# Kernel tuning notes

Measured on AMD Instinct MI355X. Metric: run time of the kernel, lower is better.

Reference implementation:

```python
import jax, jax.numpy as jnp
import numpy as np
import math

VOCAB = 32000
D = 2048
H = 16
KVH = 4
HD = D // H          # 128
FF = 5632
L = 2
S = 2048
B = 1
EPS = 1e-5
ROPE_BASE = 10000.0


def setup_inputs() -> dict:
    key = jax.random.key(0)
    ks = jax.random.split(key, 12)
    sc = 0.02
    # RoPE table: [S, HD//2, 2] (cos, sin), matching precompute_freqs_cis
    inv = 1.0 / (ROPE_BASE ** (jnp.arange(0, HD, 2, dtype=jnp.float32) / HD))
    pos = jnp.arange(S, dtype=jnp.float32)
    f = jnp.outer(pos, inv)
    freqs_cis = jnp.stack([jnp.cos(f), jnp.sin(f)], axis=-1)
    mask = jnp.tril(jnp.ones((S, S), dtype=bool))
    return {
        "input_ids": jax.random.randint(ks[0], (B, S), 0, VOCAB, dtype=jnp.int32),
        "mask": mask,
        "freqs_cis": freqs_cis,
        "w_embed": jax.random.normal(ks[1], (VOCAB, D), jnp.float32) * sc,
        "wqkv": jax.random.normal(ks[2], (L, D, D + 2 * KVH * HD), jnp.float32) * sc,
        "wo": jax.random.normal(ks[3], (L, D, D), jnp.float32) * sc,
        "w1": jax.random.normal(ks[4], (L, D, FF), jnp.float32) * sc,
        "w3": jax.random.normal(ks[5], (L, D, FF), jnp.float32) * sc,
        "w2": jax.random.normal(ks[6], (L, FF, D), jnp.float32) * sc,
        "attn_norm_w": jnp.ones((L, D), jnp.float32),
        "ff_norm_w": jnp.ones((L, D), jnp.float32),
        "final_norm_w": jnp.ones((D,), jnp.float32),
        "w_head": jax.random.normal(ks[7], (D, VOCAB), jnp.float32) * sc,
    }


def _rmsnorm(x, w):
    xf = x.astype(jnp.float32)
    n = xf * jax.lax.rsqrt(jnp.mean(xf * xf, axis=-1, keepdims=True) + EPS)
    return n.astype(x.dtype) * w


def _rope(x, fc):
    # x: [b, h, s, hd]; fc: [s, hd/2, 2]
    xr = x.reshape(*x.shape[:-1], HD // 2, 2)
    cos, sin = fc[..., 0], fc[..., 1]  # [s, hd/2] broadcast over b,h
    out = jnp.stack([xr[..., 0] * cos - xr[..., 1] * sin,
                     xr[..., 1] * cos + xr[..., 0] * sin], axis=-1)
    return out.reshape(x.shape).astype(x.dtype)


def _attention(x, mask, fc, wqkv, wo):
    b, s, _ = x.shape
    qkv = x @ wqkv  # [b, s, D + 2*kv_dim]
    kv_dim = KVH * HD
    q, k, v = jnp.split(qkv, [D, D + kv_dim], axis=-1)
    q = q.reshape(b, s, H, HD).transpose(0, 2, 1, 3)      # [b,H,s,hd]
    k = k.reshape(b, s, KVH, HD).transpose(0, 2, 1, 3)    # [b,KVH,s,hd]
    v = v.reshape(b, s, KVH, HD).transpose(0, 2, 1, 3)
    q = _rope(q, fc)
    k = _rope(k, fc)
    rep = H // KVH
    k = jnp.repeat(k, rep, axis=1)  # [b,H,s,hd]
    v = jnp.repeat(v, rep, axis=1)
    scores = jnp.einsum('bhqd,bhkd->bhqk', q, k) / math.sqrt(HD)
    scores = jnp.where(mask, scores, -1e30)
    attn = jax.nn.softmax(scores, axis=-1)
    out = jnp.einsum('bhqk,bhkd->bhqd', attn, v)
    out = out.transpose(0, 2, 1, 3).reshape(b, s, D)
    return out @ wo


def reference(input_ids, mask, freqs_cis, w_embed, wqkv, wo, w1, w3, w2,
              attn_norm_w, ff_norm_w, final_norm_w, w_head):
    x = w_embed[input_ids]  # [B,S,D]
    for l in range(L):
        h = x + _attention(_rmsnorm(x, attn_norm_w[l]), mask, freqs_cis,
                           wqkv[l], wo[l])
        hn = _rmsnorm(h, ff_norm_w[l])
        x = h + (jax.nn.silu(hn @ w1[l]) * (hn @ w3[l])) @ w2[l]
    x = _rmsnorm(x, final_norm_w)
    return x @ w_head  # [B,S,VOCAB]
```

## Files before the change

### kernel.cpp

```cpp
#include <hip/hip_runtime.h>

#define DD 2048
#define SEQ 2048
#define NH 16
#define NKV 4
#define HD 128
#define FFD 5632
#define NL 2

typedef __bf16 bf16x8 __attribute__((ext_vector_type(8)));
typedef float f32x4 __attribute__((ext_vector_type(4)));

__device__ __forceinline__ unsigned short f2bf(float f) {
    unsigned int u = __builtin_bit_cast(unsigned int, f);
    u += 0x7fffu + ((u >> 16) & 1u);
    return (unsigned short)(u >> 16);
}

__global__ __launch_bounds__(256)
void embed_gather(const int* __restrict__ ids, const float* __restrict__ wemb,
                  float* __restrict__ x)
{
    int s = blockIdx.x;
    int id = ids[s];
    const float4* src = (const float4*)(wemb + (size_t)id * DD);
    float4* dst = (float4*)(x + (size_t)s * DD);
    dst[threadIdx.x] = src[threadIdx.x];
    dst[threadIdx.x + 256] = src[threadIdx.x + 256];
}

__global__ __launch_bounds__(256)
void rmsnorm_bf16(const float* __restrict__ x, const float* __restrict__ w,
                  unsigned short* __restrict__ out)
{
    int row = blockIdx.x;
    int t = threadIdx.x;
    const float4* xr = (const float4*)(x + (size_t)row * DD);
    float4 v0 = xr[t], v1 = xr[t + 256];
    float ss = v0.x * v0.x + v0.y * v0.y + v0.z * v0.z + v0.w * v0.w
             + v1.x * v1.x + v1.y * v1.y + v1.z * v1.z + v1.w * v1.w;
#pragma unroll
    for (int off = 32; off; off >>= 1) ss += __shfl_down(ss, off);
    __shared__ float red[4];
    if ((t & 63) == 0) red[t >> 6] = ss;
    __syncthreads();
    float sc = rsqrtf((red[0] + red[1] + red[2] + red[3]) * (1.0f / DD) + 1e-5f);
    const float4* wr = (const float4*)w;
    float4 w0 = wr[t], w1v = wr[t + 256];
    ushort4 o0, o1;
    o0.x = f2bf(v0.x * sc * w0.x);  o0.y = f2bf(v0.y * sc * w0.y);
    o0.z = f2bf(v0.z * sc * w0.z);  o0.w = f2bf(v0.w * sc * w0.w);
    o1.x = f2bf(v1.x * sc * w1v.x); o1.y = f2bf(v1.y * sc * w1v.y);
    o1.z = f2bf(v1.z * sc * w1v.z); o1.w = f2bf(v1.w * sc * w1v.w);
    ushort4* op = (ushort4*)(out + (size_t)row * DD);
    op[t] = o0;
    op[t + 256] = o1;
}

__global__ __launch_bounds__(256)
void transpose_cast(const float* __restrict__ src, unsigned short* __restrict__ dst,
                    int ld_src, int ld_dst, size_t sb, size_t db)
{
    __shared__ float tile[64][65];
    src += (size_t)blockIdx.z * sb;
    dst += (size_t)blockIdx.z * db;
    int c0 = blockIdx.x * 64, r0 = blockIdx.y * 64;
    int tx = threadIdx.x & 15, ty = threadIdx.x >> 4;
#pragma unroll
    for (int i = 0; i < 4; ++i) {
        int r = ty + i * 16;
        float4 v = *(const float4*)(src + (size_t)(r0 + r) * ld_src + c0 + tx * 4);
        tile[r][tx * 4 + 0] = v.x; tile[r][tx * 4 + 1] = v.y;
        tile[r][tx * 4 + 2] = v.z; tile[r][tx * 4 + 3] = v.w;
    }
    __syncthreads();
#pragma unroll
    for (int i = 0; i < 4; ++i) {
        int c = ty + i * 16;
        ushort4 o;
        o.x = f2bf(tile[tx * 4 + 0][c]); o.y = f2bf(tile[tx * 4 + 1][c]);
        o.z = f2bf(tile[tx * 4 + 2][c]); o.w = f2bf(tile[tx * 4 + 3][c]);
        *(ushort4*)(dst + (size_t)(c0 + c) * ld_dst + r0 + tx * 4) = o;
    }
}

__global__ void rope_qk(const float* __restrict__ qkv, const float* __restrict__ fc,
                        unsigned short* __restrict__ Qb, unsigned short* __restrict__ Kb)
{
    int s = blockIdx.x;
    int hh = blockIdx.y;
    int i = threadIdx.x;
    float2 cs = *(const float2*)(fc + ((size_t)s * 64 + i) * 2);
    const float* src;
    unsigned short* dst;
    if (hh < NH) {
        src = qkv + (size_t)s * 3072 + hh * HD;
        dst = Qb + ((size_t)hh * SEQ + s) * HD;
    } else {
        int kh = hh - NH;
        src = qkv + (size_t)s * 3072 + DD + kh * HD;
        dst = Kb + ((size_t)kh * SEQ + s) * HD;
    }
    float2 xv = *(const float2*)(src + 2 * i);
    ushort2 o;
    o.x = f2bf(xv.x * cs.x - xv.y * cs.y);
    o.y = f2bf(xv.y * cs.x + xv.x * cs.y);
    *(ushort2*)(dst + 2 * i) = o;
}

__global__ __launch_bounds__(256)
void silu_mul(const float* __restrict__ h, unsigned short* __restrict__ g)
{
    size_t i = (size_t)blockIdx.x * 256 + threadIdx.x;
    size_t row = i / (FFD / 4), c4 = i % (FFD / 4);
    const float* p = h + row * (2 * FFD) + c4 * 4;
    float4 a = *(const float4*)(p);
    float4 b = *(const float4*)(p + FFD);
    ushort4 o;
    o.x = f2bf(a.x / (1.f + __expf(-a.x)) * b.x);
    o.y = f2bf(a.y / (1.f + __expf(-a.y)) * b.y);
    o.z = f2bf(a.z / (1.f + __expf(-a.z)) * b.z);
    o.w = f2bf(a.w / (1.f + __expf(-a.w)) * b.w);
    *(ushort4*)(g + row * FFD + c4 * 4) = o;
}

__global__ __launch_bounds__(256)
void gemm_bf16(const unsigned short* __restrict__ A, const unsigned short* __restrict__ B,
               float* __restrict__ C, const float* __restrict__ Res,
               int N, int K, int mT)
{
    __shared__ __attribute__((aligned(16))) unsigned char smem[65536];
    const int tid = threadIdx.x;
    const int lane = tid & 63;
    const int w = tid >> 6;
    const int nwg = gridDim.x;
    const int qq = nwg >> 3;
    const int logical = ((int)blockIdx.x & 7) * qq + ((int)blockIdx.x >> 3);
    const int m0 = (logical % mT) * 128;
    const int n0 = (logical / mT) * 128;
    const int wm = (w >> 1) * 64, wn = (w & 1) * 64;
    const int lrow = lane & 15, lgrp = lane >> 4;
    const int NT = K >> 6;

    f32x4 acc[4][4];
#pragma unroll
    for (int i = 0; i < 4; ++i)
#pragma unroll
        for (int j = 0; j < 4; ++j) acc[i][j] = 0.f;

    auto stage = [&](int bsel, int kt) {
#pragma unroll
        for (int it = 0; it < 4; ++it) {
            int o = it * 4096 + tid * 16;
            int row = o >> 7;
            int col = (o & 127) ^ ((row & 7) << 4);
            const char* ga = (const char*)A + ((size_t)(m0 + row) * K + kt) * 2 + col;
            const char* gb = (const char*)B + ((size_t)(n0 + row) * K + kt) * 2 + col;
            __builtin_amdgcn_global_load_lds(
                (__attribute__((address_space(1))) const void*)ga,
                (__attribute__((address_space(3))) void*)(smem + bsel * 32768 + it * 4096 + w * 1024),
                16, 0, 0);
            __builtin_amdgcn_global_load_lds(
                (__attribute__((address_space(1))) const void*)gb,
                (__attribute__((address_space(3))) void*)(smem + bsel * 32768 + 16384 + it * 4096 + w * 1024),
                16, 0, 0);
        }
    };

    stage(0, 0);
    int cur = 0;
    for (int t = 0; t < NT; ++t) {
        if (t + 1 < NT) {
            stage(cur ^ 1, (t + 1) << 6);
            asm volatile("s_waitcnt vmcnt(8)" ::: "memory");
        } else {
            asm volatile("s_waitcnt vmcnt(0)" ::: "memory");
        }
        __builtin_amdgcn_s_barrier();
        __builtin_amdgcn_sched_barrier(0);
        const unsigned char* buf = smem + cur * 32768;
#pragma unroll
        for (int kk = 0; kk < 2; ++kk) {
            bf16x8 af[4], bfr[4];
            int cb = kk * 64 + lgrp * 16;
#pragma unroll
            for (int i = 0; i < 4; ++i) {
                int ra = wm + i * 16 + lrow;
                af[i] = *(const bf16x8*)(buf + ra * 128 + (cb ^ ((ra & 7) << 4)));
                int rb = wn + i * 16 + lrow;
                bfr[i] = *(const bf16x8*)(buf + 16384 + rb * 128 + (cb ^ ((rb & 7) << 4)));
            }
#pragma unroll
            for (int i = 0; i < 4; ++i)
#pragma unroll
                for (int j = 0; j < 4; ++j)
                    acc[i][j] = __builtin_amdgcn_mfma_f32_16x16x32_bf16(af[i], bfr[j], acc[i][j], 0, 0, 0);
        }
        __builtin_amdgcn_s_barrier();
        cur ^= 1;
    }

    const bool hasRes = (Res != nullptr);
#pragma unroll
    for (int i = 0; i < 4; ++i)
#pragma unroll
        for (int j = 0; j < 4; ++j) {
            int r = m0 + wm + i * 16 + lgrp * 4;
            int c = n0 + wn + j * 16 + lrow;
#pragma unroll
            for (int jj = 0; jj < 4; ++jj) {
                size_t idx = (size_t)(r + jj) * N + c;
                float v = acc[i][j][jj];
                if (hasRes) v += Res[idx];
                C[idx] = v;
            }
        }
}

__global__ __launch_bounds__(512, 1)
void gemm_bf16_256(const unsigned short* __restrict__ A, const unsigned short* __restrict__ B,
                   float* __restrict__ C, int N, int K, int mT)
{
    __shared__ __attribute__((aligned(16))) unsigned char smem[131072];
    const int tid = threadIdx.x;
    const int lane = tid & 63;
    const int w = tid >> 6;
    const int nwg = gridDim.x;
    const int qq = nwg >> 3;
    const int logical = ((int)blockIdx.x & 7) * qq + ((int)blockIdx.x >> 3);
    const int m0 = (logical % mT) * 256;
    const int n0 = (logical / mT) * 256;
    const int wm2 = (w >> 2) * 128;
    const int wn4 = (w & 3) * 64;
    const int lrow = lane & 15, lgrp = lane >> 4;
    const int NT = K >> 6;

    f32x4 acc[8][4];
#pragma unroll
    for (int i = 0; i < 8; ++i)
#pragma unroll
        for (int j = 0; j < 4; ++j) acc[i][j] = 0.f;

    auto stage_all = [&](int bsel, int kt) {
#pragma unroll
        for (int it = 0; it < 8; ++it) {
            int o = (it & 3) * 8192 + tid * 16;
            int row = o >> 7;
            int col = (o & 127) ^ ((row & 7) << 4);
            const unsigned short* base = (it < 4) ? A : B;
            int r0 = (it < 4) ? m0 : n0;
            const char* g = (const char*)base + ((size_t)(r0 + row) * K + kt) * 2 + col;
            __builtin_amdgcn_global_load_lds(
                (__attribute__((address_space(1))) const void*)g,
                (__attribute__((address_space(3))) void*)(smem + bsel * 65536 +
                    (it < 4 ? 0 : 32768) + (it & 3) * 8192 + w * 1024),
                16, 0, 0);
        }
    };

    stage_all(0, 0);
    int cur = 0;
    for (int t = 0; t < NT; ++t) {
        if (t + 1 < NT) {
            stage_all(cur ^ 1, (t + 1) << 6);
            asm volatile("s_waitcnt vmcnt(8)" ::: "memory");
        } else {
            asm volatile("s_waitcnt vmcnt(0)" ::: "memory");
        }
        __builtin_amdgcn_s_barrier();
        __builtin_amdgcn_sched_barrier(0);
        const unsigned char* buf = smem + cur * 65536;

        bf16x8 bfr[4][2];
#pragma unroll
        for (int nj = 0; nj < 4; ++nj)
#pragma unroll
            for (int kk = 0; kk < 2; ++kk) {
                int rb = wn4 + nj * 16 + lrow;
                int cb = kk * 64 + lgrp * 16;
                bfr[nj][kk] = *(const bf16x8*)(buf + 32768 + rb * 128 + (cb ^ ((rb & 7) << 4)));
            }
#pragma unroll
        for (int mp = 0; mp < 4; ++mp) {
            bf16x8 afr[2][2];
#pragma unroll
            for (int i = 0; i < 2; ++i)
#pragma unroll
                for (int kk = 0; kk < 2; ++kk) {
                    int ra = wm2 + (mp * 2 + i) * 16 + lrow;
                    int cb = kk * 64 + lgrp * 16;
                    afr[i][kk] = *(const bf16x8*)(buf + ra * 128 + (cb ^ ((ra & 7) << 4)));
                }
            __builtin_amdgcn_s_setprio(1);
#pragma unroll
            for (int i = 0; i < 2; ++i)
#pragma unroll
                for (int nj = 0; nj < 4; ++nj)
#pragma unroll
                    for (int kk = 0; kk < 2; ++kk)
                        acc[mp * 2 + i][nj] = __builtin_amdgcn_mfma_f32_16x16x32_bf16(
                            afr[i][kk], bfr[nj][kk], acc[mp * 2 + i][nj], 0, 0, 0);
            __builtin_amdgcn_s_setprio(0);
        }
        __builtin_amdgcn_s_barrier();
        cur ^= 1;
    }

#pragma unroll
    for (int mi = 0; mi < 8; ++mi)
#pragma unroll
        for (int nj = 0; nj < 4; ++nj) {
            int r = m0 + wm2 + mi * 16 + lgrp * 4;
            int c = n0 + wn4 + nj * 16 + lrow;
#pragma unroll
            for (int jj = 0; jj < 4; ++jj)
                C[(size_t)(r + jj) * N + c] = acc[mi][nj][jj];
        }
}

__global__ __launch_bounds__(256)
void attn_fwd(const unsigned short* __restrict__ Qb, const unsigned short* __restrict__ Kb,
              const unsigned short* __restrict__ VTb, unsigned short* __restrict__ O)
{
    __shared__ __attribute__((aligned(16))) unsigned char smem[73728];
    const int qb = 31 - (int)blockIdx.x;
    const int h = blockIdx.y;
    const int kvh = h >> 2;
    const int tid = threadIdx.x, lane = tid & 63, w = tid >> 6;
    const int lrow = lane & 15, lgrp = lane >> 4;
    const int q0 = qb * 64 + w * 16;

    bf16x8 qf[4];
    const unsigned short* qrow = Qb + ((size_t)h * SEQ + q0 + lrow) * HD;
#pragma unroll
    for (int c = 0; c < 4; ++c)
        qf[c] = *(const bf16x8*)(qrow + c * 32 + lgrp * 8);

    float m[4], l[4];
    f32x4 oacc[8];
#pragma unroll
    for (int j = 0; j < 8; ++j) oacc[j] = 0.f;
#pragma unroll
    for (int j = 0; j < 4; ++j) { m[j] = -3.0e38f; l[j] = 0.f; }

    const float scale = 0.08838834764831845f;
    const char* kbase = (const char*)(Kb + (size_t)kvh * SEQ * HD);
    const char* vbase = (const char*)(VTb + (size_t)kvh * HD * SEQ);
    unsigned char* Pl = smem + 65536 + w * 2048;

    auto stage_kv = [&](int bsel, int t) {
#pragma unroll
        for (int it = 0; it < 4; ++it) {
            int o = it * 4096 + tid * 16;
            int row = o >> 8, col = o & 255;
            int scol = col ^ ((row & 7) << 4);
            const char* g = kbase + (size_t)(t * 64 + row) * 256 + scol;
            __builtin_amdgcn_global_load_lds(
                (__attribute__((address_space(1))) const void*)g,
                (__attribute__((address_space(3))) void*)(smem + bsel * 32768 + it * 4096 + w * 1024),
                16, 0, 0);
        }
#pragma unroll
        for (int it = 0; it < 4; ++it) {
            int o = it * 4096 + tid * 16;
            int row = o >> 7, col = o & 127;
            int scol = col ^ ((row & 7) << 4);
            const char* g = vbase + (size_t)row * (SEQ * 2) + (size_t)t * 128 + scol;
            __builtin_amdgcn_global_load_lds(
                (__attribute__((address_space(1))) const void*)g,
                (__attribute__((address_space(3))) void*)(smem + bsel * 32768 + 16384 + it * 4096 + w * 1024),
                16, 0, 0);
        }
    };

    stage_kv(0, 0);
    int cur = 0;
    for (int t = 0; t <= qb; ++t) {
        if (t < qb) {
            stage_kv(cur ^ 1, t + 1);
            asm volatile("s_waitcnt vmcnt(8)" ::: "memory");
        } else {
            asm volatile("s_waitcnt vmcnt(0)" ::: "memory");
        }
        __builtin_amdgcn_s_barrier();
        __builtin_amdgcn_sched_barrier(0);
        const unsigned char* kb = smem + cur * 32768;
        const unsigned char* vtb = kb + 16384;

        f32x4 sf[4];
#pragma unroll
        for (int kf = 0; kf < 4; ++kf) sf[kf] = 0.f;
#pragma unroll
        for (int kf = 0; kf < 4; ++kf) {
            int rb = kf * 16 + lrow;
            int rbase = rb * 256;
            int sw = (rb & 7) << 4;
#pragma unroll
            for (int c = 0; c < 4; ++c) {
                bf16x8 kfr = *(const bf16x8*)(kb + rbase + ((c * 64 + lgrp * 16) ^ sw));
                sf[kf] = __builtin_amdgcn_mfma_f32_16x16x32_bf16(qf[c], kfr, sf[kf], 0, 0, 0);
            }
        }
        const bool diag = (t == qb);
        float mx[4] = {-3.0e38f, -3.0e38f, -3.0e38f, -3.0e38f};
#pragma unroll
        for (int kf = 0; kf < 4; ++kf)
#pragma unroll
            for (int j = 0; j < 4; ++j) {
                float v = sf[kf][j] * scale;
                if (diag && (t * 64 + kf * 16 + lrow) > (q0 + lgrp * 4 + j)) v = -3.0e38f;
                sf[kf][j] = v;
                mx[j] = fmaxf(mx[j], v);
            }
#pragma unroll
        for (int off = 1; off < 16; off <<= 1)
#pragma unroll
            for (int j = 0; j < 4; ++j) mx[j] = fmaxf(mx[j], __shfl_xor(mx[j], off));
        float alpha[4], rs[4];
#pragma unroll
        for (int j = 0; j < 4; ++j) {
            float mn = fmaxf(m[j], mx[j]);
            alpha[j] = __expf(m[j] - mn);
            m[j] = mn;
            rs[j] = 0.f;
        }
#pragma unroll
        for (int kf = 0; kf < 4; ++kf)
#pragma unroll
            for (int j = 0; j < 4; ++j) {
                float p = __expf(sf[kf][j] - m[j]);
                rs[j] += p;
                int qq = lgrp * 4 + j;
                int addr = qq * 128 + (((kf * 16 + lrow) * 2) ^ ((qq & 7) << 4));
                *(unsigned short*)(Pl + addr) = f2bf(p);
            }
#pragma unroll
        for (int off = 1; off < 16; off <<= 1)
#pragma unroll
            for (int j = 0; j < 4; ++j) rs[j] += __shfl_xor(rs[j], off);
#pragma unroll
        for (int j = 0; j < 4; ++j) l[j] = l[j] * alpha[j] + rs[j];
#pragma unroll
        for (int hf = 0; hf < 8; ++hf)
#pragma unroll
            for (int j = 0; j < 4; ++j) oacc[hf][j] *= alpha[j];
#pragma unroll
        for (int c = 0; c < 2; ++c) {
            int cb = c * 64 + lgrp * 16;
            bf16x8 pf = *(const bf16x8*)(Pl + lrow * 128 + (cb ^ ((lrow & 7) << 4)));
#pragma unroll
            for (int hf = 0; hf < 8; ++hf) {
                int rv = hf * 16 + lrow;
                bf16x8 vf = *(const bf16x8*)(vtb + rv * 128 + (cb ^ ((rv & 7) << 4)));
                oacc[hf] = __builtin_amdgcn_mfma_f32_16x16x32_bf16(pf, vf, oacc[hf], 0, 0, 0);
            }
        }
        __builtin_amdgcn_s_barrier();
        cur ^= 1;
    }
#pragma unroll
    for (int hf = 0; hf < 8; ++hf)
#pragma unroll
        for (int j = 0; j < 4; ++j) {
            float v = oacc[hf][j] / l[j];
            int qg = q0 + lgrp * 4 + j;
            O[(size_t)qg * DD + h * HD + hf * 16 + lrow] = f2bf(v);
        }
}

extern "C" void kernel_launch(void* const* d_in, const int* in_sizes, int n_in,
                              void* d_out, int out_size, void* d_ws, size_t ws_size,
                              hipStream_t stream)
{
    (void)in_sizes; (void)n_in; (void)out_size; (void)ws_size;
    const int* ids = (const int*)d_in[0];
    const float* fc   = (const float*)d_in[2];
    const float* wemb = (const float*)d_in[3];
    const float* wqkv = (const float*)d_in[4];
    const float* wo   = (const float*)d_in[5];
    const float* w1   = (const float*)d_in[6];
    const float* w3   = (const float*)d_in[7];
    const float* w2   = (const float*)d_in[8];
    const float* anw  = (const float*)d_in[9];
    const float* fnw  = (const float*)d_in[10];
    const float* finw = (const float*)d_in[11];
    const float* wh   = (const float*)d_in[12];
    float* out = (float*)d_out;
    char* ws = (char*)d_ws;

    unsigned short* WQKVT = (unsigned short*)(ws);
    unsigned short* WOT   = (unsigned short*)(ws + 25165824);
    unsigned short* W13T  = (unsigned short*)(ws + 41943040);
    unsigned short* W2T   = (unsigned short*)(ws + 134217728);
    unsigned short* WHT   = (unsigned short*)(ws + 180355072);
    float*          X     = (float*)(ws + 311427072);
    unsigned short* XN    = (unsigned short*)(ws + 328204288);
    float*          QKV   = (float*)(ws + 336592896);
    unsigned short* Qb    = (unsigned short*)(ws + 361758720);
    unsigned short* Kb    = (unsigned short*)(ws + 370147328);
    unsigned short* VT    = (unsigned short*)(ws + 372244480);
    unsigned short* AO    = (unsigned short*)(ws + 374341632);
    float*          H13   = (float*)(ws + 382730240);
    unsigned short* G     = (unsigned short*)(ws + 475004928);

    transpose_cast<<<dim3(48, 32, 2), 256, 0, stream>>>(wqkv, WQKVT, 3072, 2048,
        (size_t)2048 * 3072, (size_t)3072 * 2048);
    transpose_cast<<<dim3(32, 32, 2), 256, 0, stream>>>(wo, WOT, 2048, 2048,
        (size_t)2048 * 2048, (size_t)2048 * 2048);
    transpose_cast<<<dim3(88, 32, 2), 256, 0, stream>>>(w1, W13T, 5632, 2048,
        (size_t)2048 * 5632, (size_t)11264 * 2048);
    transpose_cast<<<dim3(88, 32, 2), 256, 0, stream>>>(w3, W13T + (size_t)5632 * 2048, 5632, 2048,
        (size_t)2048 * 5632, (size_t)11264 * 2048);
    transpose_cast<<<dim3(32, 88, 2), 256, 0, stream>>>(w2, W2T, 2048, 5632,
        (size_t)5632 * 2048, (size_t)2048 * 5632);
    transpose_cast<<<dim3(500, 32, 1), 256, 0, stream>>>(wh, WHT, 32000, 2048, 0, 0);

    embed_gather<<<dim3(SEQ), 256, 0, stream>>>(ids, wemb, X);

    for (int lyr = 0; lyr < NL; ++lyr) {
        const unsigned short* wqkvT_l = WQKVT + (size_t)lyr * 3072 * 2048;
        const unsigned short* woT_l   = WOT   + (size_t)lyr * 2048 * 2048;
        const unsigned short* w13T_l  = W13T  + (size_t)lyr * 11264 * 2048;
        const unsigned short* w2T_l   = W2T   + (size_t)lyr * 2048 * 5632;

        rmsnorm_bf16<<<dim3(SEQ), 256, 0, stream>>>(X, anw + lyr * DD, XN);
        gemm_bf16<<<dim3(24 * 16), 256, 0, stream>>>(XN, wqkvT_l, QKV, nullptr, 3072, 2048, 16);
        rope_qk<<<dim3(SEQ, NH + NKV), 64, 0, stream>>>(QKV, fc, Qb, Kb);
        transpose_cast<<<dim3(2, 32, 4), 256, 0, stream>>>(QKV + 2560, VT, 3072, 2048,
            128, (size_t)128 * 2048);
        attn_fwd<<<dim3(32, NH), 256, 0, stream>>>(Qb, Kb, VT, AO);
        gemm_bf16<<<dim3(16 * 16), 256, 0, stream>>>(AO, woT_l, X, X, 2048, 2048, 16);
        rmsnorm_bf16<<<dim3(SEQ), 256, 0, stream>>>(X, fnw + lyr * DD, XN);
        gemm_bf16_256<<<dim3(8 * 44), 512, 0, stream>>>(XN, w13T_l, H13, 11264, 2048, 8);
        silu_mul<<<dim3(11264), 256, 0, stream>>>(H13, G);
        gemm_bf16<<<dim3(16 * 16), 256, 0, stream>>>(G, w2T_l, X, X, 2048, 5632, 16);
    }
    rmsnorm_bf16<<<dim3(SEQ), 256, 0, stream>>>(X, finw, XN);
    gemm_bf16_256<<<dim3(8 * 125), 512, 0, stream>>>(XN, WHT, out, 32000, 2048, 8);
}
```

Baseline: 1.283 ms.

## Restructure 256-tile GEMM into four-stage K=32 pipeline with split staging

The 256x256 bf16 GEMM main loop changes from a double-buffered K=64 tile to a four-buffer K=32 ring with three tiles in flight. A and B loads are issued separately, with B loads placed in the middle of the compute phase, and a new LDS swizzle packs two rows per 128-byte line. A second barrier splits the MFMA work into two halves. The goal is deeper prefetch and better overlap of global-to-LDS traffic with MFMA work, at the cost of more barriers per K-step and trickier vmcnt bookkeeping.

Result: no change. 1.276 ms (-0.5%).

```diff
diff --git a/kernel.cpp b/kernel.cpp
--- a/kernel.cpp
+++ b/kernel.cpp
@@ -10,6 +10,9 @@
 
 typedef __bf16 bf16x8 __attribute__((ext_vector_type(8)));
 typedef float f32x4 __attribute__((ext_vector_type(4)));
+
+#define AS1 __attribute__((address_space(1)))
+#define AS3 __attribute__((address_space(3)))
 
 __device__ __forceinline__ unsigned short f2bf(float f) {
     unsigned int u = __builtin_bit_cast(unsigned int, f);
@@ -157,12 +160,12 @@
             const char* ga = (const char*)A + ((size_t)(m0 + row) * K + kt) * 2 + col;
             const char* gb = (const char*)B + ((size_t)(n0 + row) * K + kt) * 2 + col;
             __builtin_amdgcn_global_load_lds(
-                (__attribute__((address_space(1))) const void*)ga,
-                (__attribute__((address_space(3))) void*)(smem + bsel * 32768 + it * 4096 + w * 1024),
+                (AS1 const void*)ga,
+                (AS3 void*)(smem + bsel * 32768 + it * 4096 + w * 1024),
                 16, 0, 0);
             __builtin_amdgcn_global_load_lds(
-                (__attribute__((address_space(1))) const void*)gb,
-                (__attribute__((address_space(3))) void*)(smem + bsel * 32768 + 16384 + it * 4096 + w * 1024),
+                (AS1 const void*)gb,
+                (AS3 void*)(smem + bsel * 32768 + 16384 + it * 4096 + w * 1024),
                 16, 0, 0);
         }
     };
@@ -231,9 +234,8 @@
     const int m0 = (logical % mT) * 256;
     const int n0 = (logical / mT) * 256;
     const int wm2 = (w >> 2) * 128;
-    const int wn4 = (w & 3) * 64;
-    const int lrow = lane & 15, lgrp = lane >> 4;
-    const int NT = K >> 6;
+    const int lrow = lane & 15, lgrp = (lane >> 4) & 3;
+    const int NT = K >> 5;
 
     f32x4 acc[8][4];
 #pragma unroll
@@ -241,69 +243,69 @@
 #pragma unroll
         for (int j = 0; j < 4; ++j) acc[i][j] = 0.f;
 
-    auto stage_all = [&](int bsel, int kt) {
-#pragma unroll
-        for (int it = 0; it < 8; ++it) {
-            int o = (it & 3) * 8192 + tid * 16;
-            int row = o >> 7;
-            int col = (o & 127) ^ ((row & 7) << 4);
-            const unsigned short* base = (it < 4) ? A : B;
-            int r0 = (it < 4) ? m0 : n0;
-            const char* g = (const char*)base + ((size_t)(r0 + row) * K + kt) * 2 + col;
+    const int X = (((lrow & 1) << 6) | (lgrp << 4)) ^ ((lrow >> 1) << 4);
+    const int aoff = ((wm2 >> 1) + (lrow >> 1)) * 128 + X;
+    const int boff = 16384 + (((w & 3) * 32) + (lrow >> 1)) * 128 + X;
+
+    auto stage_part = [&](int ktile, int part) {
+        const unsigned short* base = part ? B : A;
+        const int r0 = part ? n0 : m0;
+        const int ktb = ktile << 6;
+#pragma unroll
+        for (int j = 0; j < 2; ++j) {
+            int o = j * 8192 + tid * 16;
+            int p = o >> 7;
+            int sl = (o & 127) ^ ((p & 7) << 4);
+            int r = 2 * p + (sl >> 6);
+            int cb = sl & 63;
+            const char* g = (const char*)base + (size_t)(r0 + r) * K * 2 + ktb + cb;
             __builtin_amdgcn_global_load_lds(
-                (__attribute__((address_space(1))) const void*)g,
-                (__attribute__((address_space(3))) void*)(smem + bsel * 65536 +
-                    (it < 4 ? 0 : 32768) + (it & 3) * 8192 + w * 1024),
+                (AS1 const void*)g,
+                (AS3 void*)(smem + (ktile & 3) * 32768 + part * 16384 + o),
                 16, 0, 0);
         }
     };
 
-    stage_all(0, 0);
-    int cur = 0;
+#pragma unroll
+    for (int p0 = 0; p0 < 3; ++p0) { stage_part(p0, 0); stage_part(p0, 1); }
+
     for (int t = 0; t < NT; ++t) {
-        if (t + 1 < NT) {
-            stage_all(cur ^ 1, (t + 1) << 6);
-            asm volatile("s_waitcnt vmcnt(8)" ::: "memory");
-        } else {
-            asm volatile("s_waitcnt vmcnt(0)" ::: "memory");
-        }
+        const unsigned char* buf = smem + (t & 3) * 32768;
+        const bool have3 = (t + 3 < NT);
+        if (have3) stage_part(t + 3, 0);
+        if (have3)              asm volatile("s_waitcnt vmcnt(10)" ::: "memory");
+        else if (t + 2 < NT)    asm volatile("s_waitcnt vmcnt(8)"  ::: "memory");
+        else if (t + 1 < NT)    asm volatile("s_waitcnt vmcnt(4)"  ::: "memory");
+        else                    asm volatile("s_waitcnt vmcnt(0)"  ::: "memory");
         __builtin_amdgcn_s_barrier();
         __builtin_amdgcn_sched_barrier(0);
-        const unsigned char* buf = smem + cur * 65536;
-
-        bf16x8 bfr[4][2];
-#pragma unroll
-        for (int nj = 0; nj < 4; ++nj)
-#pragma unroll
-            for (int kk = 0; kk < 2; ++kk) {
-                int rb = wn4 + nj * 16 + lrow;
-                int cb = kk * 64 + lgrp * 16;
-                bfr[nj][kk] = *(const bf16x8*)(buf + 32768 + rb * 128 + (cb ^ ((rb & 7) << 4)));
-            }
-#pragma unroll
-        for (int mp = 0; mp < 4; ++mp) {
-            bf16x8 afr[2][2];
-#pragma unroll
-            for (int i = 0; i < 2; ++i)
-#pragma unroll
-                for (int kk = 0; kk < 2; ++kk) {
-                    int ra = wm2 + (mp * 2 + i) * 16 + lrow;
-                    int cb = kk * 64 + lgrp * 16;
-                    afr[i][kk] = *(const bf16x8*)(buf + ra * 128 + (cb ^ ((ra & 7) << 4)));
-                }
-            __builtin_amdgcn_s_setprio(1);
-#pragma unroll
-            for (int i = 0; i < 2; ++i)
-#pragma unroll
-                for (int nj = 0; nj < 4; ++nj)
-#pragma unroll
-                    for (int kk = 0; kk < 2; ++kk)
-                        acc[mp * 2 + i][nj] = __builtin_amdgcn_mfma_f32_16x16x32_bf16(
-                            afr[i][kk], bfr[nj][kk], acc[mp * 2 + i][nj], 0, 0, 0);
-            __builtin_amdgcn_s_setprio(0);
-        }
+        bf16x8 bfr[4], afr[4];
+#pragma unroll
+        for (int nj = 0; nj < 4; ++nj) bfr[nj] = *(const bf16x8*)(buf + boff + nj * 1024);
+#pragma unroll
+        for (int mi = 0; mi < 4; ++mi) afr[mi] = *(const bf16x8*)(buf + aoff + mi * 1024);
+        __builtin_amdgcn_s_setprio(1);
+#pragma unroll
+        for (int mi = 0; mi < 4; ++mi)
+#pragma unroll
+            for (int nj = 0; nj < 4; ++nj)
+                acc[mi][nj] = __builtin_amdgcn_mfma_f32_16x16x32_bf16(afr[mi], bfr[nj], acc[mi][nj], 0, 0, 0);
+        __builtin_amdgcn_s_setprio(0);
+        bf16x8 afr2[4];
+#pragma unroll
+        for (int mi = 0; mi < 4; ++mi) afr2[mi] = *(const bf16x8*)(buf + aoff + (mi + 4) * 1024);
+        if (have3) stage_part(t + 3, 1);
+        asm volatile("s_waitcnt lgkmcnt(0)" ::: "memory");
+        __builtin_amdgcn_sched_barrier(0);
         __builtin_amdgcn_s_barrier();
-        cur ^= 1;
+        __builtin_amdgcn_sched_barrier(0);
+        __builtin_amdgcn_s_setprio(1);
+#pragma unroll
+        for (int mi = 0; mi < 4; ++mi)
+#pragma unroll
+            for (int nj = 0; nj < 4; ++nj)
+                acc[mi + 4][nj] = __builtin_amdgcn_mfma_f32_16x16x32_bf16(afr2[mi], bfr[nj], acc[mi + 4][nj], 0, 0, 0);
+        __builtin_amdgcn_s_setprio(0);
     }
 
 #pragma unroll
@@ -311,7 +313,7 @@
 #pragma unroll
         for (int nj = 0; nj < 4; ++nj) {
             int r = m0 + wm2 + mi * 16 + lgrp * 4;
-            int c = n0 + wn4 + nj * 16 + lrow;
+            int c = n0 + (w & 3) * 64 + nj * 16 + lrow;
 #pragma unroll
             for (int jj = 0; jj < 4; ++jj)
                 C[(size_t)(r + jj) * N + c] = acc[mi][nj][jj];
@@ -356,8 +358,8 @@
             int scol = col ^ ((row & 7) << 4);
             const char* g = kbase + (size_t)(t * 64 + row) * 256 + scol;
             __builtin_amdgcn_global_load_lds(
-                (__attribute__((address_space(1))) const void*)g,
-                (__attribute__((address_space(3))) void*)(smem + bsel * 32768 + it * 4096 + w * 1024),
+                (AS1 const void*)g,
+                (AS3 void*)(smem + bsel * 32768 + it * 4096 + w * 1024),
                 16, 0, 0);
         }
 #pragma unroll
@@ -367,8 +369,8 @@
             int scol = col ^ ((row & 7) << 4);
             const char* g = vbase + (size_t)row * (SEQ * 2) + (size_t)t * 128 + scol;
             __builtin_amdgcn_global_load_lds(
-                (__attribute__((address_space(1))) const void*)g,
-                (__attribute__((address_space(3))) void*)(smem + bsel * 32768 + 16384 + it * 4096 + w * 1024),
+                (AS1 const void*)g,
+                (AS3 void*)(smem + bsel * 32768 + 16384 + it * 4096 + w * 1024),
                 16, 0, 0);
         }
     };
```
